# Kernel optimization log

Measured on AMD Instinct MI355X. Metric: run time of the kernel, lower is better.

## Reference

```python
import jax, jax.numpy as jnp
import numpy as np

SCALE = 0.08838834764831845  # 1/sqrt(128)
NEG_INF = -1e30


def setup_inputs() -> dict:
    key = jax.random.key(0)
    ks = jax.random.split(key, 6)
    S, Hq, Hkv, D, NB, BS, BMAX, X = 32, 32, 8, 128, 4096, 16, 128, 8
    query = jax.random.normal(ks[0], (S, Hq, D), jnp.float32)
    key_cache = jax.random.normal(ks[1], (NB, Hkv, D // X, BS, X), jnp.float32)
    value_cache = jax.random.normal(ks[2], (NB, Hkv, D, BS), jnp.float32)
    block_tables = jax.random.randint(ks[3], (S, BMAX), 0, NB, dtype=jnp.int32)
    seq_lens = jax.random.randint(ks[4], (S,), 1, BMAX * BS + 1, dtype=jnp.int32)
    alibi_slopes = jax.random.uniform(ks[5], (Hq,), jnp.float32)
    query_start_len = jnp.arange(S + 1, dtype=jnp.int32)  # every seq is a 1-token decode
    return dict(query_ptr=query, key_cache_ptr=key_cache, value_cache_ptr=value_cache,
                block_tables_ptr=block_tables, seq_lens_ptr=seq_lens,
                alibi_slopes_ptr=alibi_slopes, query_start_len_ptr=query_start_len)


def reference(query_ptr, key_cache_ptr, value_cache_ptr, block_tables_ptr,
              seq_lens_ptr, alibi_slopes_ptr, query_start_len_ptr):
    S, Bmax = block_tables_ptr.shape
    NB, Hkv, D0, BS, X = key_cache_ptr.shape
    D = D0 * X
    Hq = query_ptr.shape[1]
    G = Hq // Hkv  # queries per kv head
    Kmax = Bmax * BS

    # de-interleave vLLM K layout [NB,Hkv,D//x,BS,x] -> [NB,Hkv,BS,D]; K[d] = cache[.., d//x, tok, d%x]
    K = key_cache_ptr.transpose(0, 1, 3, 2, 4).reshape(NB, Hkv, BS, D).astype(jnp.float32)
    V = value_cache_ptr.transpose(0, 1, 3, 2).astype(jnp.float32)  # [NB,Hkv,BS,D]

    qstart = query_start_len_ptr[:-1]
    qlen = query_start_len_ptr[1:] - qstart

    q = query_ptr[qstart].astype(jnp.float32).reshape(S, Hkv, G, D)  # one decode token per seq

    # block-table-driven KV gather: [S,Bmax,Hkv,BS,D] -> [S,Hkv,Kmax,D]
    Kg = K[block_tables_ptr].transpose(0, 2, 1, 3, 4).reshape(S, Hkv, Kmax, D)
    Vg = V[block_tables_ptr].transpose(0, 2, 1, 3, 4).reshape(S, Hkv, Kmax, D)

    scores = SCALE * jnp.einsum('shgd,shkd->shgk', q, Kg)  # [S,Hkv,G,Kmax]

    pos = jnp.arange(Kmax, dtype=jnp.float32)
    ctx = (seq_lens_ptr.astype(jnp.float32) - 1.0)[:, None, None, None]
    slopes = alibi_slopes_ptr.reshape(Hkv, G)  # head idx = kv_head*G + q
    bias = slopes[None, :, :, None] * (pos[None, None, None, :] - ctx)
    valid = (jnp.arange(Kmax)[None, :] < seq_lens_ptr[:, None])[:, None, None, :]
    scores = jnp.where(valid, scores + bias, NEG_INF)

    m = jnp.max(scores, axis=-1, keepdims=True)
    p = jnp.exp(scores - m) * valid  # online-softmax numerator
    l = jnp.sum(p, axis=-1, keepdims=True)
    acc = jnp.einsum('shgk,shkd->shgd', p, Vg)
    out = acc / (l + 1e-10)  # matches acc/(L + 1e-10) in source

    decode = (qlen == 1).astype(query_ptr.dtype)  # seqs with query_len>1 are skipped (zeros)
    out = out.reshape(S, Hq, D).astype(query_ptr.dtype) * decode[:, None, None]
    return jnp.zeros_like(query_ptr).at[qstart].set(out)
```

## Files before the change

### kernel.cpp

```cpp
#include <hip/hip_runtime.h>

#define SCALE_F 0.08838834764831845f
#define NEG_INF -1e30f

constexpr int S    = 32;
constexpr int Hq   = 32;
constexpr int Hkv  = 8;
constexpr int G    = 4;
constexpr int D    = 128;
constexpr int BS   = 16;
constexpr int BMAX = 128;
constexpr int KMAX = BMAX * BS;

template<int PARTS>
__global__ __launch_bounds__(256, 6)
void attn_part_kernel(const float* __restrict__ q_ptr,
                      const float* __restrict__ kc,
                      const float* __restrict__ vc,
                      const int*   __restrict__ bt,
                      const int*   __restrict__ slens,
                      const float* __restrict__ slopes,
                      float* __restrict__ part_acc,
                      float* __restrict__ part_m,
                      float* __restrict__ part_l)
{
    constexpr int CHUNK = KMAX / PARTS;
    constexpr int CPB   = CHUNK / BS;

    __shared__ float sm_s[G * CHUNK];
    __shared__ float sm_acc[G * D];

    const int bid  = blockIdx.x;
    const int part = bid % PARTS;
    const int sh   = bid / PARTS;
    const int h    = sh % Hkv;
    const int s    = sh / Hkv;

    const int seq_len   = slens[s];
    const int num_parts = (seq_len + CHUNK - 1) / CHUNK;
    if (part >= num_parts) return;

    const int tid       = threadIdx.x;
    const int kvb0      = part * CPB;
    const int nb_total  = (seq_len + BS - 1) / BS;
    const int cpb_valid = min(CPB, nb_total - kvb0);
    const int lim       = cpb_valid * BS;

    float slope[G];
    #pragma unroll
    for (int g = 0; g < G; ++g) slope[g] = slopes[h * G + g];
    const float ctx = (float)(seq_len - 1);

    int phys[CPB];
    #pragma unroll
    for (int i = 0; i < CPB; ++i) phys[i] = bt[s * BMAX + kvb0 + i];

    const int o = tid >> 4;
    const int t = tid & 15;

    float4 qa[G], qb[G];
    #pragma unroll
    for (int g = 0; g < G; ++g) {
        const float* qp = q_ptr + ((size_t)(s * Hq + h * G + g) * D + t * 8);
        qa[g] = ((const float4*)qp)[0];
        qb[g] = ((const float4*)qp)[1];
    }

    float4 ka, kb, nka, nkb;
    {
        const float* kp = kc + ((((size_t)phys[0] * Hkv + h) * (D / 8) + t) * BS + o) * 8;
        ka = ((const float4*)kp)[0];
        kb = ((const float4*)kp)[1];
    }
    #pragma unroll
    for (int i = 0; i < CPB; ++i) {
        if (i >= cpb_valid) break;
        if (i + 1 < cpb_valid) {
            const float* kp = kc + ((((size_t)phys[i + 1] * Hkv + h) * (D / 8) + t) * BS + o) * 8;
            nka = ((const float4*)kp)[0];
            nkb = ((const float4*)kp)[1];
        }
        float sc[G];
        #pragma unroll
        for (int g = 0; g < G; ++g)
            sc[g] = qa[g].x * ka.x + qa[g].y * ka.y + qa[g].z * ka.z + qa[g].w * ka.w
                  + qb[g].x * kb.x + qb[g].y * kb.y + qb[g].z * kb.z + qb[g].w * kb.w;
        #pragma unroll
        for (int g = 0; g < G; ++g) {
            #pragma unroll
            for (int msk = 8; msk >= 1; msk >>= 1)
                sc[g] += __shfl_xor(sc[g], msk, 16);
        }
        const int kpos  = (kvb0 + i) * BS + o;
        const bool valid = kpos < seq_len;
        if (t == 0) {
            #pragma unroll
            for (int g = 0; g < G; ++g)
                sm_s[g * CHUNK + i * BS + o] =
                    valid ? (SCALE_F * sc[g] + slope[g] * ((float)kpos - ctx)) : NEG_INF;
        }
        ka = nka; kb = nkb;
    }
    __syncthreads();

    {
        const int g    = tid >> 6;
        const int lane = tid & 63;
        float m = NEG_INF;
        for (int j = lane; j < lim; j += 64) m = fmaxf(m, sm_s[g * CHUNK + j]);
        #pragma unroll
        for (int msk = 32; msk >= 1; msk >>= 1) m = fmaxf(m, __shfl_xor(m, msk, 64));
        float l = 0.f;
        for (int j = lane; j < lim; j += 64) {
            float p = __expf(sm_s[g * CHUNK + j] - m);
            sm_s[g * CHUNK + j] = p;
            l += p;
        }
        #pragma unroll
        for (int msk = 32; msk >= 1; msk >>= 1) l += __shfl_xor(l, msk, 64);
        if (lane == 0) {
            part_m[(sh * PARTS + part) * G + g] = m;
            part_l[(sh * PARTS + part) * G + g] = l;
        }
    }
    __syncthreads();

    const int d    = tid & 127;
    const int half = tid >> 7;
    float acc[G] = {0.f, 0.f, 0.f, 0.f};

    float4 v0, v1, v2, v3, w0, w1, w2, w3;
    if (half < cpb_valid) {
        const float* vp = vc + (((size_t)phys[half] * Hkv + h) * D + d) * BS;
        v0 = ((const float4*)vp)[0]; v1 = ((const float4*)vp)[1];
        v2 = ((const float4*)vp)[2]; v3 = ((const float4*)vp)[3];
    }
    for (int i = half; i < cpb_valid; i += 2) {
        if (i + 2 < cpb_valid) {
            const float* vp = vc + (((size_t)phys[i + 2] * Hkv + h) * D + d) * BS;
            w0 = ((const float4*)vp)[0]; w1 = ((const float4*)vp)[1];
            w2 = ((const float4*)vp)[2]; w3 = ((const float4*)vp)[3];
        }
        #pragma unroll
        for (int g = 0; g < G; ++g) {
            const float4* pp = (const float4*)(sm_s + g * CHUNK + i * BS);
            float4 p0 = pp[0], p1 = pp[1], p2 = pp[2], p3 = pp[3];
            acc[g] += p0.x * v0.x + p0.y * v0.y + p0.z * v0.z + p0.w * v0.w;
            acc[g] += p1.x * v1.x + p1.y * v1.y + p1.z * v1.z + p1.w * v1.w;
            acc[g] += p2.x * v2.x + p2.y * v2.y + p2.z * v2.z + p2.w * v2.w;
            acc[g] += p3.x * v3.x + p3.y * v3.y + p3.z * v3.z + p3.w * v3.w;
        }
        v0 = w0; v1 = w1; v2 = w2; v3 = w3;
    }
    if (half == 1) {
        #pragma unroll
        for (int g = 0; g < G; ++g) sm_acc[g * D + d] = acc[g];
    }
    __syncthreads();
    if (half == 0) {
        float* outp = part_acc + (size_t)(sh * PARTS + part) * G * D;
        #pragma unroll
        for (int g = 0; g < G; ++g)
            outp[g * D + d] = acc[g] + sm_acc[g * D + d];
    }
}

__global__ __launch_bounds__(512)
void attn_reduce_kernel(const float* __restrict__ part_acc,
                        const float* __restrict__ part_m,
                        const float* __restrict__ part_l,
                        const int*   __restrict__ slens,
                        float* __restrict__ out,
                        int parts, int chunk)
{
    const int sh  = blockIdx.x;
    const int s   = sh / Hkv;
    const int tid = threadIdx.x;
    const int g   = tid >> 7;
    const int d   = tid & 127;

    const int seq_len = slens[s];
    const int np = min(parts, (seq_len + chunk - 1) / chunk);

    float M = NEG_INF;
    for (int p = 0; p < np; ++p)
        M = fmaxf(M, part_m[(sh * parts + p) * G + g]);
    float L = 0.f, acc = 0.f;
    for (int p = 0; p < np; ++p) {
        const float w = __expf(part_m[(sh * parts + p) * G + g] - M);
        L += w * part_l[(sh * parts + p) * G + g];
        acc += w * part_acc[((size_t)(sh * parts + p) * G + g) * D + d];
    }
    out[(size_t)(sh * G + g) * D + d] = acc / (L + 1e-10f);
}

extern "C" void kernel_launch(void* const* d_in, const int* in_sizes, int n_in,
                              void* d_out, int out_size, void* d_ws, size_t ws_size,
                              hipStream_t stream)
{
    const float* q   = (const float*)d_in[0];
    const float* kc  = (const float*)d_in[1];
    const float* vc  = (const float*)d_in[2];
    const int*   bt  = (const int*)d_in[3];
    const int*   sl  = (const int*)d_in[4];
    const float* slp = (const float*)d_in[5];

    auto ws_need = [](int p) {
        return (size_t)S * Hkv * p * G * (D + 2) * sizeof(float);
    };
    int parts = 16;
    while (parts > 1 && ws_need(parts) > ws_size) parts >>= 1;
    const int chunk = KMAX / parts;

    float* part_acc = (float*)d_ws;
    float* part_m   = part_acc + (size_t)S * Hkv * parts * G * D;
    float* part_l   = part_m   + (size_t)S * Hkv * parts * G;

    const dim3 grid1(S * Hkv * parts);
    switch (parts) {
    case 16: attn_part_kernel<16><<<grid1, 256, 0, stream>>>(q, kc, vc, bt, sl, slp, part_acc, part_m, part_l); break;
    case 8:  attn_part_kernel<8> <<<grid1, 256, 0, stream>>>(q, kc, vc, bt, sl, slp, part_acc, part_m, part_l); break;
    case 4:  attn_part_kernel<4> <<<grid1, 256, 0, stream>>>(q, kc, vc, bt, sl, slp, part_acc, part_m, part_l); break;
    case 2:  attn_part_kernel<2> <<<grid1, 256, 0, stream>>>(q, kc, vc, bt, sl, slp, part_acc, part_m, part_l); break;
    default: attn_part_kernel<1> <<<grid1, 256, 0, stream>>>(q, kc, vc, bt, sl, slp, part_acc, part_m, part_l); break;
    }
    attn_reduce_kernel<<<S * Hkv, 512, 0, stream>>>(
        part_acc, part_m, part_l, sl, (float*)d_out, parts, chunk);
}
```

Before: 476.6 us.

## Split KV into more parts and batch K/V loads ahead of softmax

New measurement: 477.4 us. No clear change (+0.2%).

```diff
diff --git a/kernel.cpp b/kernel.cpp
--- a/kernel.cpp
+++ b/kernel.cpp
@@ -13,7 +13,7 @@
 constexpr int KMAX = BMAX * BS;
 
 template<int PARTS>
-__global__ __launch_bounds__(256, 6)
+__global__ __launch_bounds__(256, 4)
 void attn_part_kernel(const float* __restrict__ q_ptr,
                       const float* __restrict__ kc,
                       const float* __restrict__ vc,
@@ -40,11 +40,8 @@
     const int num_parts = (seq_len + CHUNK - 1) / CHUNK;
     if (part >= num_parts) return;
 
-    const int tid       = threadIdx.x;
-    const int kvb0      = part * CPB;
-    const int nb_total  = (seq_len + BS - 1) / BS;
-    const int cpb_valid = min(CPB, nb_total - kvb0);
-    const int lim       = cpb_valid * BS;
+    const int tid  = threadIdx.x;
+    const int kvb0 = part * CPB;
 
     float slope[G];
     #pragma unroll
@@ -55,8 +52,8 @@
     #pragma unroll
     for (int i = 0; i < CPB; ++i) phys[i] = bt[s * BMAX + kvb0 + i];
 
-    const int o = tid >> 4;
-    const int t = tid & 15;
+    const int oo = tid >> 4;
+    const int t  = tid & 15;
 
     float4 qa[G], qb[G];
     #pragma unroll
@@ -66,52 +63,65 @@
         qb[g] = ((const float4*)qp)[1];
     }
 
-    float4 ka, kb, nka, nkb;
-    {
-        const float* kp = kc + ((((size_t)phys[0] * Hkv + h) * (D / 8) + t) * BS + o) * 8;
-        ka = ((const float4*)kp)[0];
-        kb = ((const float4*)kp)[1];
-    }
-    #pragma unroll
-    for (int i = 0; i < CPB; ++i) {
-        if (i >= cpb_valid) break;
-        if (i + 1 < cpb_valid) {
-            const float* kp = kc + ((((size_t)phys[i + 1] * Hkv + h) * (D / 8) + t) * BS + o) * 8;
-            nka = ((const float4*)kp)[0];
-            nkb = ((const float4*)kp)[1];
-        }
-        float sc[G];
-        #pragma unroll
-        for (int g = 0; g < G; ++g)
-            sc[g] = qa[g].x * ka.x + qa[g].y * ka.y + qa[g].z * ka.z + qa[g].w * ka.w
-                  + qb[g].x * kb.x + qb[g].y * kb.y + qb[g].z * kb.z + qb[g].w * kb.w;
-        #pragma unroll
-        for (int g = 0; g < G; ++g) {
-            #pragma unroll
-            for (int msk = 8; msk >= 1; msk >>= 1)
-                sc[g] += __shfl_xor(sc[g], msk, 16);
-        }
-        const int kpos  = (kvb0 + i) * BS + o;
-        const bool valid = kpos < seq_len;
-        if (t == 0) {
+    #pragma unroll
+    for (int i0 = 0; i0 < CPB; i0 += 4) {
+        float4 ka[4], kb[4];
+        #pragma unroll
+        for (int u = 0; u < 4; ++u) {
+            const float* kp = kc + ((((size_t)phys[i0 + u] * Hkv + h) * (D / 8) + t) * BS + oo) * 8;
+            ka[u] = ((const float4*)kp)[0];
+            kb[u] = ((const float4*)kp)[1];
+        }
+        #pragma unroll
+        for (int u = 0; u < 4; ++u) {
+            const int i = i0 + u;
+            float sc[G];
             #pragma unroll
             for (int g = 0; g < G; ++g)
-                sm_s[g * CHUNK + i * BS + o] =
-                    valid ? (SCALE_F * sc[g] + slope[g] * ((float)kpos - ctx)) : NEG_INF;
-        }
-        ka = nka; kb = nkb;
-    }
+                sc[g] = qa[g].x * ka[u].x + qa[g].y * ka[u].y + qa[g].z * ka[u].z + qa[g].w * ka[u].w
+                      + qb[g].x * kb[u].x + qb[g].y * kb[u].y + qb[g].z * kb[u].z + qb[g].w * kb[u].w;
+            #pragma unroll
+            for (int g = 0; g < G; ++g) {
+                #pragma unroll
+                for (int msk = 8; msk >= 1; msk >>= 1)
+                    sc[g] += __shfl_xor(sc[g], msk, 16);
+            }
+            const int kpos   = (kvb0 + i) * BS + oo;
+            const bool valid = kpos < seq_len;
+            if (t == 0) {
+                #pragma unroll
+                for (int g = 0; g < G; ++g)
+                    sm_s[g * CHUNK + i * BS + oo] =
+                        valid ? (SCALE_F * sc[g] + slope[g] * ((float)kpos - ctx)) : NEG_INF;
+            }
+        }
+    }
+
+    const int d    = tid & 127;
+    const int half = tid >> 7;
+    float4 v[2][4];
+    #pragma unroll
+    for (int j = 0; j < 2 && half + 2 * j < CPB; ++j) {
+        const float* vp = vc + (((size_t)phys[half + 2 * j] * Hkv + h) * D + d) * BS;
+        v[j][0] = ((const float4*)vp)[0];
+        v[j][1] = ((const float4*)vp)[1];
+        v[j][2] = ((const float4*)vp)[2];
+        v[j][3] = ((const float4*)vp)[3];
+    }
+
     __syncthreads();
 
     {
         const int g    = tid >> 6;
         const int lane = tid & 63;
         float m = NEG_INF;
-        for (int j = lane; j < lim; j += 64) m = fmaxf(m, sm_s[g * CHUNK + j]);
+        #pragma unroll
+        for (int j = lane; j < CHUNK; j += 64) m = fmaxf(m, sm_s[g * CHUNK + j]);
         #pragma unroll
         for (int msk = 32; msk >= 1; msk >>= 1) m = fmaxf(m, __shfl_xor(m, msk, 64));
         float l = 0.f;
-        for (int j = lane; j < lim; j += 64) {
+        #pragma unroll
+        for (int j = lane; j < CHUNK; j += 64) {
             float p = __expf(sm_s[g * CHUNK + j] - m);
             sm_s[g * CHUNK + j] = p;
             l += p;
@@ -125,32 +135,27 @@
     }
     __syncthreads();
 
-    const int d    = tid & 127;
-    const int half = tid >> 7;
     float acc[G] = {0.f, 0.f, 0.f, 0.f};
-
-    float4 v0, v1, v2, v3, w0, w1, w2, w3;
-    if (half < cpb_valid) {
-        const float* vp = vc + (((size_t)phys[half] * Hkv + h) * D + d) * BS;
-        v0 = ((const float4*)vp)[0]; v1 = ((const float4*)vp)[1];
-        v2 = ((const float4*)vp)[2]; v3 = ((const float4*)vp)[3];
-    }
-    for (int i = half; i < cpb_valid; i += 2) {
-        if (i + 2 < cpb_valid) {
-            const float* vp = vc + (((size_t)phys[i + 2] * Hkv + h) * D + d) * BS;
-            w0 = ((const float4*)vp)[0]; w1 = ((const float4*)vp)[1];
-            w2 = ((const float4*)vp)[2]; w3 = ((const float4*)vp)[3];
-        }
+    #pragma unroll
+    for (int jj = 0; jj < CPB / 2; ++jj) {
+        const int i = half + 2 * jj;
+        const int b = jj & 1;
         #pragma unroll
         for (int g = 0; g < G; ++g) {
             const float4* pp = (const float4*)(sm_s + g * CHUNK + i * BS);
             float4 p0 = pp[0], p1 = pp[1], p2 = pp[2], p3 = pp[3];
-            acc[g] += p0.x * v0.x + p0.y * v0.y + p0.z * v0.z + p0.w * v0.w;
-            acc[g] += p1.x * v1.x + p1.y * v1.y + p1.z * v1.z + p1.w * v1.w;
-            acc[g] += p2.x * v2.x + p2.y * v2.y + p2.z * v2.z + p2.w * v2.w;
-            acc[g] += p3.x * v3.x + p3.y * v3.y + p3.z * v3.z + p3.w * v3.w;
-        }
-        v0 = w0; v1 = w1; v2 = w2; v3 = w3;
+            acc[g] += p0.x * v[b][0].x + p0.y * v[b][0].y + p0.z * v[b][0].z + p0.w * v[b][0].w;
+            acc[g] += p1.x * v[b][1].x + p1.y * v[b][1].y + p1.z * v[b][1].z + p1.w * v[b][1].w;
+            acc[g] += p2.x * v[b][2].x + p2.y * v[b][2].y + p2.z * v[b][2].z + p2.w * v[b][2].w;
+            acc[g] += p3.x * v[b][3].x + p3.y * v[b][3].y + p3.z * v[b][3].z + p3.w * v[b][3].w;
+        }
+        if (i + 4 < CPB) {
+            const float* vp = vc + (((size_t)phys[i + 4] * Hkv + h) * D + d) * BS;
+            v[b][0] = ((const float4*)vp)[0];
+            v[b][1] = ((const float4*)vp)[1];
+            v[b][2] = ((const float4*)vp)[2];
+            v[b][3] = ((const float4*)vp)[3];
+        }
     }
     if (half == 1) {
         #pragma unroll
@@ -208,8 +213,8 @@
     auto ws_need = [](int p) {
         return (size_t)S * Hkv * p * G * (D + 2) * sizeof(float);
     };
-    int parts = 16;
-    while (parts > 1 && ws_need(parts) > ws_size) parts >>= 1;
+    int parts = 32;
+    while (parts > 4 && ws_need(parts) > ws_size) parts >>= 1;
     const int chunk = KMAX / parts;
 
     float* part_acc = (float*)d_ws;
@@ -218,11 +223,9 @@
 
     const dim3 grid1(S * Hkv * parts);
     switch (parts) {
+    case 32: attn_part_kernel<32><<<grid1, 256, 0, stream>>>(q, kc, vc, bt, sl, slp, part_acc, part_m, part_l); break;
     case 16: attn_part_kernel<16><<<grid1, 256, 0, stream>>>(q, kc, vc, bt, sl, slp, part_acc, part_m, part_l); break;
-    case 8:  attn_part_kernel<8> <<<grid1, 256, 0, stream>>>(q, kc, vc, bt, sl, slp, part_acc, part_m, part_l); break;
-    case 4:  attn_part_kernel<4> <<<grid1, 256, 0, stream>>>(q, kc, vc, bt, sl, slp, part_acc, part_m, part_l); break;
-    case 2:  attn_part_kernel<2> <<<grid1, 256, 0, stream>>>(q, kc, vc, bt, sl, slp, part_acc, part_m, part_l); break;
-    default: attn_part_kernel<1> <<<grid1, 256, 0, stream>>>(q, kc, vc, bt, sl, slp, part_acc, part_m, part_l); break;
+    default: attn_part_kernel<8> <<<grid1, 256, 0, stream>>>(q, kc, vc, bt, sl, slp, part_acc, part_m, part_l); break;
     }
     attn_reduce_kernel<<<S * Hkv, 512, 0, stream>>>(
         part_acc, part_m, part_l, sl, (float*)d_out, parts, chunk);
```
